# Performance work log

Hardware: AMD Instinct MI355X
Metric: run time of the kernel (lower is better)

Reference implementation:

```python
import jax, jax.numpy as jnp
import numpy as np

K = 10
ALPHA = 0.1

def setup_inputs() -> dict:
    key = jax.random.key(0)
    k1, k2, k3, k4 = jax.random.split(key, 4)
    N, E, IN, HID, OUT = 100000, 3200000, 512, 256, 64
    x = jax.random.normal(k1, (N, IN), dtype=jnp.float32)
    edge_index = jax.random.randint(k2, (2, E), 0, N, dtype=jnp.int64)
    W1 = jax.random.normal(k3, (IN, HID), dtype=jnp.float32) * (1.0 / np.sqrt(IN))
    b1 = jnp.zeros((HID,), jnp.float32)
    W2 = jax.random.normal(k4, (HID, OUT), dtype=jnp.float32) * (1.0 / np.sqrt(HID))
    b2 = jnp.zeros((OUT,), jnp.float32)
    return {"x": x, "edge_index": edge_index, "W1": W1, "b1": b1, "W2": W2, "b2": b2}

def reference(x, edge_index, W1, b1, W2, b2):
    N = x.shape[0]
    # gcn_norm with self-loops (PyG default for APPNP)
    loop = jnp.arange(N, dtype=edge_index.dtype)
    src = jnp.concatenate([edge_index[0], loop])  # [E+N]
    dst = jnp.concatenate([edge_index[1], loop])
    ones = jnp.ones(src.shape[0], dtype=x.dtype)
    deg = jax.ops.segment_sum(ones, dst, num_segments=N)
    dis = jnp.where(deg > 0, jax.lax.rsqrt(deg), 0.0)
    norm = dis[src] * dis[dst]  # [E+N]

    # 2-layer MLP (dropout disabled: eval mode)
    h = jnp.maximum(x @ W1 + b1, 0.0) @ W2 + b2  # [N, out]

    # K-step PPR diffusion: z <- alpha*h + (1-alpha)*A_hat z
    def step(z, _):
        agg = jax.ops.segment_sum(norm[:, None] * z[src], dst, num_segments=N)
        return ALPHA * h + (1.0 - ALPHA) * agg, None

    z, _ = jax.lax.scan(step, h, None, length=K)
    return jax.nn.log_softmax(z, axis=-1)
```

## Files before the change

### kernel.cpp

```cpp
#include <hip/hip_runtime.h>
#include <hip/hip_bf16.h>

#define ALPHA_F 0.1f
#define KSTEPS 10
#define BKT_SH 9
#define P1_CHUNK 8192
#define MAXPAD_PER_BUCKET (512 * 32)

typedef __attribute__((ext_vector_type(8))) short bf16x8;
typedef __attribute__((ext_vector_type(4))) float f32x4;

__device__ __forceinline__ unsigned short f2bf(float f) {
  union { float f; unsigned int u; } v; v.f = f;
  unsigned int u = v.u;
  u += 0x7FFFu + ((u >> 16) & 1u);
  return (unsigned short)(u >> 16);
}
__device__ __forceinline__ float bflo(unsigned int u) { return __uint_as_float(u << 16); }
__device__ __forceinline__ float bfhi(unsigned int u) { return __uint_as_float(u & 0xFFFF0000u); }

__device__ __forceinline__ void gload16(const void* g, void* l) {
  __builtin_amdgcn_global_load_lds(
      (const __attribute__((address_space(1))) void*)g,
      (__attribute__((address_space(3))) void*)l, 16, 0, 0);
}


__global__ __launch_bounds__(256)
void p0_hist(const int* __restrict__ dstv, int E, int* __restrict__ bhist) {
  __shared__ int h[256];
  int t = threadIdx.x;
  h[t] = 0;
  __syncthreads();
  int b0 = blockIdx.x * P1_CHUNK;
  int lim = min(P1_CHUNK, E - b0);
  for (int i = t; i < lim; i += 256) atomicAdd(&h[dstv[b0 + i] >> BKT_SH], 1);
  __syncthreads();
  if (h[t]) atomicAdd(&bhist[t], h[t]);
}

__global__ void p0_scan(const int* __restrict__ bhist, int* __restrict__ bbase,
                        int* __restrict__ gcur) {
  __shared__ int s[256];
  int t = threadIdx.x;
  int mine = bhist[t];
  s[t] = mine;
  __syncthreads();
  for (int off = 1; off < 256; off <<= 1) {
    int v = (t >= off) ? s[t - off] : 0;
    __syncthreads();
    s[t] += v;
    __syncthreads();
  }
  int excl = s[t] - mine;
  bbase[t] = excl;
  gcur[t] = excl;
}

__global__ __launch_bounds__(256)
void p1_scatter(const int* __restrict__ srcv, const int* __restrict__ dstv, int E,
                int* __restrict__ gcur, int2* __restrict__ tmp) {
  __shared__ int h[256];
  __shared__ int loc[256];
  int t = threadIdx.x;
  int b0 = blockIdx.x * P1_CHUNK;
  int lim = min(P1_CHUNK, E - b0);
  h[t] = 0;
  __syncthreads();
  for (int i = t; i < lim; i += 256) atomicAdd(&h[dstv[b0 + i] >> BKT_SH], 1);
  __syncthreads();
  loc[t] = h[t] ? atomicAdd(&gcur[t], h[t]) : 0;
  __syncthreads();
  h[t] = 0;
  __syncthreads();
  for (int i = t; i < lim; i += 256) {
    int d = dstv[b0 + i], s = srcv[b0 + i];
    int b = d >> BKT_SH;
    int pos = loc[b] + atomicAdd(&h[b], 1);
    tmp[pos] = make_int2(s, d);
  }
}

__global__ __launch_bounds__(256)
void p2_bucket(const int2* __restrict__ tmp, const int* __restrict__ bbase,
               const int* __restrict__ bhist, int* __restrict__ counts,
               int* __restrict__ rowptr, int* __restrict__ col, int N) {
  __shared__ int h1[512];
  __shared__ int cur[512];
  __shared__ int s2[256];
  const int t = threadIdx.x;
  const int b = blockIdx.x;
  const int base = bbase[b];
  const int pbase = base + b * MAXPAD_PER_BUCKET;
  const int sz = bhist[b];
  const int r0 = b << BKT_SH;
  const int nrows = min(512, N - r0);

  h1[t] = 0; h1[t + 256] = 0;
  __syncthreads();
  for (int i = t; i < sz; i += 256) atomicAdd(&h1[tmp[base + i].y - r0], 1);
  __syncthreads();
  int a = (h1[2 * t] + 31) & ~31;
  int c = (h1[2 * t + 1] + 31) & ~31;
  s2[t] = a + c;
  __syncthreads();
  for (int off = 1; off < 256; off <<= 1) {
    int v = (t >= off) ? s2[t - off] : 0;
    __syncthreads();
    s2[t] += v;
    __syncthreads();
  }
  int excl2 = s2[t] - (a + c);
  cur[2 * t] = excl2;
  cur[2 * t + 1] = excl2 + a;
  __syncthreads();
  if (t < nrows)       { rowptr[r0 + t] = pbase + cur[t];             counts[r0 + t] = h1[t]; }
  if (t + 256 < nrows) { rowptr[r0 + t + 256] = pbase + cur[t + 256]; counts[r0 + t + 256] = h1[t + 256]; }
  __syncthreads();
  for (int i = t; i < sz; i += 256) {
    int2 e = tmp[base + i];
    int p = pbase + atomicAdd(&cur[e.y - r0], 1);
    col[p] = e.x;
  }
  __syncthreads();
  for (int i = t; i < nrows; i += 256) {
    int cnt = h1[i];
    int c32 = (cnt + 31) & ~31;
    int ps = pbase + cur[i];
    for (int k = cnt; k < c32; ++k) col[ps++] = N;
  }
}

__global__ void k_dis(const int* __restrict__ counts, float* __restrict__ dis, int N) {
  int i = blockIdx.x * 256 + threadIdx.x;
  if (i < N) dis[i] = rsqrtf((float)(counts[i] + 1));
}

__global__ void k_zrow(unsigned short* __restrict__ yA, unsigned short* __restrict__ yB, int N) {
  int t = threadIdx.x;
  if (t < 64) yA[(size_t)N * 64 + t] = 0;
  else        yB[(size_t)N * 64 + (t - 64)] = 0;
}

__global__ void k_wconv1(const float* __restrict__ W, unsigned short* __restrict__ WT) {
  int idx = blockIdx.x * 256 + threadIdx.x;
  if (idx >= 512 * 256) return;
  int e = idx & 7, n = (idx >> 3) & 15, q = (idx >> 7) & 7;
  int nsub = (idx >> 10) & 15, kstep = idx >> 14;
  int k = kstep * 64 + q * 8 + e;
  int ncol = nsub * 16 + n;
  WT[idx] = f2bf(W[(size_t)k * 256 + ncol]);
}

__global__ void k_wconv2(const float* __restrict__ W, unsigned short* __restrict__ WT) {
  int idx = blockIdx.x * 256 + threadIdx.x;
  if (idx >= 256 * 64) return;
  int e = idx & 7, n = (idx >> 3) & 15, q = (idx >> 7) & 7;
  int nsub = (idx >> 10) & 3, kstep = idx >> 12;
  int k = kstep * 64 + q * 8 + e;
  int ncol = nsub * 16 + n;
  WT[idx] = f2bf(W[(size_t)k * 64 + ncol]);
}

__global__ __launch_bounds__(512)
void gemm1_kernel(const float* __restrict__ X, const unsigned short* __restrict__ Bt,
                  const float* __restrict__ bias, unsigned short* __restrict__ outT,
                  int M) {
  __shared__ __align__(16) unsigned short Al[8192];
  __shared__ __align__(16) unsigned short Bl[16384];
  const int t = threadIdx.x;
  const int m0 = blockIdx.x * 128;
  const int lane = t & 63;
  const int w = t >> 6;
  const int wm = w >> 2, wn = w & 3;

  const int sm = ((t >> 7) << 4) + (t & 15);
  const int sq = (t >> 4) & 7;
  const int r1 = m0 + sm;
  const int r2 = r1 + 64;
  const bool g1 = r1 < M, g2 = r2 < M;

  f32x4 acc[4][4] = {};

  for (int ks = 0; ks < 8; ++ks) {
    const int kc = ks * 64 + sq * 8;
    uint4 v1 = {0, 0, 0, 0}, v2 = {0, 0, 0, 0};
    if (g1) {
      const float* p = X + (size_t)r1 * 512 + kc;
      float4 a = *(const float4*)p, b = *(const float4*)(p + 4);
      unsigned short* o = (unsigned short*)&v1;
      o[0] = f2bf(a.x); o[1] = f2bf(a.y); o[2] = f2bf(a.z); o[3] = f2bf(a.w);
      o[4] = f2bf(b.x); o[5] = f2bf(b.y); o[6] = f2bf(b.z); o[7] = f2bf(b.w);
    }
    if (g2) {
      const float* p = X + (size_t)r2 * 512 + kc;
      float4 a = *(const float4*)p, b = *(const float4*)(p + 4);
      unsigned short* o = (unsigned short*)&v2;
      o[0] = f2bf(a.x); o[1] = f2bf(a.y); o[2] = f2bf(a.z); o[3] = f2bf(a.w);
      o[4] = f2bf(b.x); o[5] = f2bf(b.y); o[6] = f2bf(b.z); o[7] = f2bf(b.w);
    }
    *(uint4*)&Al[t * 8] = v1;
    *(uint4*)&Al[(t + 512) * 8] = v2;

    const unsigned short* bs = Bt + ks * 16384;
    gload16(bs + (size_t)t * 8,          &Bl[t * 8]);
    gload16(bs + (size_t)(t + 512) * 8,  &Bl[(t + 512) * 8]);
    gload16(bs + (size_t)(t + 1024) * 8, &Bl[(t + 1024) * 8]);
    gload16(bs + (size_t)(t + 1536) * 8, &Bl[(t + 1536) * 8]);
    __syncthreads();

#pragma unroll
    for (int kk = 0; kk < 2; ++kk) {
      bf16x8 af[4], bfv[4];
#pragma unroll
      for (int mi = 0; mi < 4; ++mi)
        af[mi] = *(const bf16x8*)&Al[((wm * 4 + mi) * 128 + kk * 64 + (lane >> 4) * 16 + (lane & 15)) * 8];
#pragma unroll
      for (int ni = 0; ni < 4; ++ni)
        bfv[ni] = *(const bf16x8*)&Bl[((wn * 4 + ni) * 128 + kk * 64 + (lane >> 4) * 16 + (lane & 15)) * 8];
#pragma unroll
      for (int mi = 0; mi < 4; ++mi)
#pragma unroll
        for (int ni = 0; ni < 4; ++ni)
          acc[mi][ni] = __builtin_amdgcn_mfma_f32_16x16x32_bf16(af[mi], bfv[ni], acc[mi][ni], 0, 0, 0);
    }
    __syncthreads();
  }

  unsigned short* ob = outT + (size_t)blockIdx.x * 32768;
#pragma unroll
  for (int mi = 0; mi < 4; ++mi) {
#pragma unroll
    for (int ni = 0; ni < 4; ++ni) {
      int n = wn * 64 + ni * 16 + (lane & 15);
      float bv = bias[n];
      int kstep = n >> 6, q = (n >> 3) & 7, e = n & 7;
#pragma unroll
      for (int j = 0; j < 4; ++j) {
        int lm = wm * 64 + mi * 16 + (lane >> 4) * 4 + j;
        if (m0 + lm < M) {
          float v = fmaxf(acc[mi][ni][j] + bv, 0.f);
          int msub = lm >> 4, mm = lm & 15;
          ob[((((kstep * 8 + msub) * 8 + q) * 16 + mm) * 8) + e] = f2bf(v);
        }
      }
    }
  }
}

__global__ __launch_bounds__(256)
void gemm2_kernel(const unsigned short* __restrict__ At, const unsigned short* __restrict__ Bt,
                  const float* __restrict__ bias, const float* __restrict__ dis,
                  unsigned short* __restrict__ hb, unsigned short* __restrict__ y0, int M) {
  __shared__ __align__(16) unsigned short Al[8192];
  __shared__ __align__(16) unsigned short Bl[4096];
  const int t = threadIdx.x;
  const int m0 = blockIdx.x * 128;
  const int lane = t & 63;
  const int w = t >> 6;
  const int wm = w >> 1, wn = w & 1;

  f32x4 acc[4][2] = {};

  const unsigned short* ab = At + (size_t)blockIdx.x * 32768;
  for (int ks = 0; ks < 4; ++ks) {
    const unsigned short* as = ab + ks * 8192;
    gload16(as + (size_t)t * 8,         &Al[t * 8]);
    gload16(as + (size_t)(t + 256) * 8, &Al[(t + 256) * 8]);
    gload16(as + (size_t)(t + 512) * 8, &Al[(t + 512) * 8]);
    gload16(as + (size_t)(t + 768) * 8, &Al[(t + 768) * 8]);
    const unsigned short* bs = Bt + ks * 4096;
    gload16(bs + (size_t)t * 8,         &Bl[t * 8]);
    gload16(bs + (size_t)(t + 256) * 8, &Bl[(t + 256) * 8]);
    __syncthreads();

#pragma unroll
    for (int kk = 0; kk < 2; ++kk) {
      bf16x8 af[4], bfv[2];
#pragma unroll
      for (int mi = 0; mi < 4; ++mi)
        af[mi] = *(const bf16x8*)&Al[((wm * 4 + mi) * 128 + kk * 64 + (lane >> 4) * 16 + (lane & 15)) * 8];
#pragma unroll
      for (int ni = 0; ni < 2; ++ni)
        bfv[ni] = *(const bf16x8*)&Bl[((wn * 2 + ni) * 128 + kk * 64 + (lane >> 4) * 16 + (lane & 15)) * 8];
#pragma unroll
      for (int mi = 0; mi < 4; ++mi)
#pragma unroll
        for (int ni = 0; ni < 2; ++ni)
          acc[mi][ni] = __builtin_amdgcn_mfma_f32_16x16x32_bf16(af[mi], bfv[ni], acc[mi][ni], 0, 0, 0);
    }
    __syncthreads();
  }

#pragma unroll
  for (int mi = 0; mi < 4; ++mi) {
#pragma unroll
    for (int ni = 0; ni < 2; ++ni) {
      int gn = wn * 32 + ni * 16 + (lane & 15);
      float bv = bias[gn];
#pragma unroll
      for (int j = 0; j < 4; ++j) {
        int gm = m0 + wm * 64 + mi * 16 + (lane >> 4) * 4 + j;
        if (gm < M) {
          float v = acc[mi][ni][j] + bv;
          hb[(size_t)gm * 64 + gn] = f2bf(v);
          y0[(size_t)gm * 64 + gn] = f2bf(dis[gm] * v);
        }
      }
    }
  }
}

template<bool FINAL>
__global__ __launch_bounds__(256)
void prop_kernel(const unsigned short* __restrict__ yin,
                 const unsigned short* __restrict__ hb,
                 void* __restrict__ yout,
                 const int* __restrict__ rowptr, const int* __restrict__ counts,
                 const int* __restrict__ col, const float* __restrict__ dis, int N) {
  int wid = (blockIdx.x * 256 + threadIdx.x) >> 6;
  wid = __builtin_amdgcn_readfirstlane(wid);
  if (wid >= N) return;
  const int lane = threadIdx.x & 63;
  const int g = lane >> 3;
  const int lg = lane & 7;
  const int r = wid;

  const int start = rowptr[r];
  const int cnt = counts[r];
  const int iters = (cnt + 31) >> 5;
  const float dr = dis[r];
  uint4 zs = *(const uint4*)(yin + (size_t)r * 64 + 8 * lg);
  uint4 hr = *(const uint4*)(hb + (size_t)r * 64 + 8 * lg);

  float acc[8] = {0.f, 0.f, 0.f, 0.f, 0.f, 0.f, 0.f, 0.f};
  const int* cp = col + start + 4 * g;
  for (int it = 0; it < iters; ++it, cp += 32) {
    int4 cc = *(const int4*)cp;
    uint4 z0 = *(const uint4*)(yin + (size_t)cc.x * 64 + 8 * lg);
    uint4 z1 = *(const uint4*)(yin + (size_t)cc.y * 64 + 8 * lg);
    uint4 z2 = *(const uint4*)(yin + (size_t)cc.z * 64 + 8 * lg);
    uint4 z3 = *(const uint4*)(yin + (size_t)cc.w * 64 + 8 * lg);
    acc[0] += bflo(z0.x); acc[1] += bfhi(z0.x); acc[2] += bflo(z0.y); acc[3] += bfhi(z0.y);
    acc[4] += bflo(z0.z); acc[5] += bfhi(z0.z); acc[6] += bflo(z0.w); acc[7] += bfhi(z0.w);
    acc[0] += bflo(z1.x); acc[1] += bfhi(z1.x); acc[2] += bflo(z1.y); acc[3] += bfhi(z1.y);
    acc[4] += bflo(z1.z); acc[5] += bfhi(z1.z); acc[6] += bflo(z1.w); acc[7] += bfhi(z1.w);
    acc[0] += bflo(z2.x); acc[1] += bfhi(z2.x); acc[2] += bflo(z2.y); acc[3] += bfhi(z2.y);
    acc[4] += bflo(z2.z); acc[5] += bfhi(z2.z); acc[6] += bflo(z2.w); acc[7] += bfhi(z2.w);
    acc[0] += bflo(z3.x); acc[1] += bfhi(z3.x); acc[2] += bflo(z3.y); acc[3] += bfhi(z3.y);
    acc[4] += bflo(z3.z); acc[5] += bfhi(z3.z); acc[6] += bflo(z3.w); acc[7] += bfhi(z3.w);
  }
#pragma unroll
  for (int k = 0; k < 8; ++k) {
    acc[k] += __shfl_xor(acc[k], 8);
    acc[k] += __shfl_xor(acc[k], 16);
    acc[k] += __shfl_xor(acc[k], 32);
  }

  float selfz[8] = { bflo(zs.x), bfhi(zs.x), bflo(zs.y), bfhi(zs.y),
                     bflo(zs.z), bfhi(zs.z), bflo(zs.w), bfhi(zs.w) };
  float hv[8]    = { bflo(hr.x), bfhi(hr.x), bflo(hr.y), bfhi(hr.y),
                     bflo(hr.z), bfhi(hr.z), bflo(hr.w), bfhi(hr.w) };
  float f[8];
#pragma unroll
  for (int k = 0; k < 8; ++k)
    f[k] = ALPHA_F * hv[k] + (1.f - ALPHA_F) * dr * (acc[k] + selfz[k]);

  if (!FINAL) {
    if (g == 0) {
      uint4 o;
      o.x = (unsigned)f2bf(dr * f[0]) | ((unsigned)f2bf(dr * f[1]) << 16);
      o.y = (unsigned)f2bf(dr * f[2]) | ((unsigned)f2bf(dr * f[3]) << 16);
      o.z = (unsigned)f2bf(dr * f[4]) | ((unsigned)f2bf(dr * f[5]) << 16);
      o.w = (unsigned)f2bf(dr * f[6]) | ((unsigned)f2bf(dr * f[7]) << 16);
      *(uint4*)((unsigned short*)yout + (size_t)r * 64 + 8 * lg) = o;
    }
  } else {
    float m = f[0];
#pragma unroll
    for (int k = 1; k < 8; ++k) m = fmaxf(m, f[k]);
    m = fmaxf(m, __shfl_xor(m, 1));
    m = fmaxf(m, __shfl_xor(m, 2));
    m = fmaxf(m, __shfl_xor(m, 4));
    float s = 0.f;
#pragma unroll
    for (int k = 0; k < 8; ++k) s += __expf(f[k] - m);
    s += __shfl_xor(s, 1);
    s += __shfl_xor(s, 2);
    s += __shfl_xor(s, 4);
    float ls = __logf(s);
    if (g == 0) {
      float* op = (float*)yout + (size_t)r * 64 + 8 * lg;
      *(float4*)op       = make_float4(f[0] - m - ls, f[1] - m - ls, f[2] - m - ls, f[3] - m - ls);
      *(float4*)(op + 4) = make_float4(f[4] - m - ls, f[5] - m - ls, f[6] - m - ls, f[7] - m - ls);
    }
  }
}

extern "C" void kernel_launch(void* const* d_in, const int* in_sizes, int n_in,
                              void* d_out, int out_size, void* d_ws, size_t ws_size,
                              hipStream_t stream) {
  const float* x  = (const float*)d_in[0];
  const int*   ei = (const int*)d_in[1];
  const float* W1 = (const float*)d_in[2];
  const float* b1 = (const float*)d_in[3];
  const float* W2 = (const float*)d_in[4];
  const float* b2 = (const float*)d_in[5];

  const int IN = 512, HID = 256, OUT = 64;
  const int N = in_sizes[0] / IN;
  const int E = in_sizes[1] / 2;
  const int* srcv = ei;
  const int* dstv = ei + E;
  const int NBUCK = (N + (1 << BKT_SH) - 1) >> BKT_SH;
  const int MT = (N + 127) / 128;
  const size_t N1 = (size_t)N + 1;

  char* p = (char*)d_ws;
  auto alloc = [&](size_t bytes) -> void* {
    void* r = (void*)p;
    p += (bytes + 255) & ~(size_t)255;
    return r;
  };
  int*   bhist  = (int*)alloc(256 * 4);
  int*   bbase  = (int*)alloc(256 * 4);
  int*   gcur   = (int*)alloc(256 * 4);
  int*   counts = (int*)alloc((size_t)N * 4);
  float* dis    = (float*)alloc((size_t)N * 4);
  int*   rowptr = (int*)alloc((size_t)(N + 1) * 4);
  int*   col    = (int*)alloc(((size_t)E + 256 * MAXPAD_PER_BUCKET) * 4);
  unsigned short* WT1t = (unsigned short*)alloc((size_t)IN * HID * 2);
  unsigned short* WT2t = (unsigned short*)alloc((size_t)HID * OUT * 2);
  unsigned short* hb   = (unsigned short*)alloc((size_t)N * OUT * 2);
  unsigned short* yA   = (unsigned short*)alloc(N1 * OUT * 2);
  size_t hidT_bytes = (size_t)MT * 32768 * 2;
  size_t R_bytes = hidT_bytes;
  if ((size_t)E * 8 > R_bytes) R_bytes = (size_t)E * 8;
  if (N1 * OUT * 2 > R_bytes) R_bytes = N1 * OUT * 2;
  char* R = (char*)alloc(R_bytes);
  int2* tmp = (int2*)R;
  unsigned short* hidT = (unsigned short*)R;
  unsigned short* yB = (unsigned short*)R;

  hipMemsetAsync(bhist, 0, 256 * 4, stream);

  const int p1blocks = (E + P1_CHUNK - 1) / P1_CHUNK;
  p0_hist<<<p1blocks, 256, 0, stream>>>(dstv, E, bhist);
  p0_scan<<<1, 256, 0, stream>>>(bhist, bbase, gcur);
  p1_scatter<<<p1blocks, 256, 0, stream>>>(srcv, dstv, E, gcur, tmp);
  p2_bucket<<<NBUCK, 256, 0, stream>>>(tmp, bbase, bhist, counts, rowptr, col, N);
  k_dis<<<(N + 255) / 256, 256, 0, stream>>>(counts, dis, N);

  k_wconv1<<<(IN * HID + 255) / 256, 256, 0, stream>>>(W1, WT1t);
  k_wconv2<<<(HID * OUT + 255) / 256, 256, 0, stream>>>(W2, WT2t);

  gemm1_kernel<<<MT, 512, 0, stream>>>(x, WT1t, b1, hidT, N);
  gemm2_kernel<<<MT, 256, 0, stream>>>(hidT, WT2t, b2, dis, hb, yA, N);
  k_zrow<<<1, 128, 0, stream>>>(yA, yB, N);

  const int pblocks = (N + 3) / 4;
  const unsigned short* ycur = yA;
  for (int it = 0; it < KSTEPS - 1; ++it) {
    unsigned short* ynext = (it & 1) ? yA : yB;
    prop_kernel<false><<<pblocks, 256, 0, stream>>>(ycur, hb, ynext, rowptr, counts, col, dis, N);
    ycur = ynext;
  }
  prop_kernel<true><<<pblocks, 256, 0, stream>>>(ycur, hb, d_out, rowptr, counts, col, dis, N);
}
```

Before: 764.8 us.

## Split feature dim into XCD-local halves, pack edge temp, fuse dis into bucketing

```diff
diff --git a/kernel.cpp b/kernel.cpp
--- a/kernel.cpp
+++ b/kernel.cpp
@@ -5,7 +5,7 @@
 #define KSTEPS 10
 #define BKT_SH 9
 #define P1_CHUNK 8192
-#define MAXPAD_PER_BUCKET (512 * 32)
+#define MAXPAD_PER_BUCKET (512 * 16)
 
 typedef __attribute__((ext_vector_type(8))) short bf16x8;
 typedef __attribute__((ext_vector_type(4))) float f32x4;
@@ -59,7 +59,7 @@
 
 __global__ __launch_bounds__(256)
 void p1_scatter(const int* __restrict__ srcv, const int* __restrict__ dstv, int E,
-                int* __restrict__ gcur, int2* __restrict__ tmp) {
+                int* __restrict__ gcur, int* __restrict__ tmp) {
   __shared__ int h[256];
   __shared__ int loc[256];
   int t = threadIdx.x;
@@ -77,14 +77,15 @@
     int d = dstv[b0 + i], s = srcv[b0 + i];
     int b = d >> BKT_SH;
     int pos = loc[b] + atomicAdd(&h[b], 1);
-    tmp[pos] = make_int2(s, d);
-  }
-}
-
-__global__ __launch_bounds__(256)
-void p2_bucket(const int2* __restrict__ tmp, const int* __restrict__ bbase,
+    tmp[pos] = (s << BKT_SH) | (d & 511);
+  }
+}
+
+__global__ __launch_bounds__(256)
+void p2_bucket(const int* __restrict__ tmp, const int* __restrict__ bbase,
                const int* __restrict__ bhist, int* __restrict__ counts,
-               int* __restrict__ rowptr, int* __restrict__ col, int N) {
+               float* __restrict__ dis, int* __restrict__ rowptr,
+               int* __restrict__ col, int N) {
   __shared__ int h1[512];
   __shared__ int cur[512];
   __shared__ int s2[256];
@@ -98,10 +99,10 @@
 
   h1[t] = 0; h1[t + 256] = 0;
   __syncthreads();
-  for (int i = t; i < sz; i += 256) atomicAdd(&h1[tmp[base + i].y - r0], 1);
-  __syncthreads();
-  int a = (h1[2 * t] + 31) & ~31;
-  int c = (h1[2 * t + 1] + 31) & ~31;
+  for (int i = t; i < sz; i += 256) atomicAdd(&h1[tmp[base + i] & 511], 1);
+  __syncthreads();
+  int a = (h1[2 * t] + 15) & ~15;
+  int c = (h1[2 * t + 1] + 15) & ~15;
   s2[t] = a + c;
   __syncthreads();
   for (int off = 1; off < 256; off <<= 1) {
@@ -114,32 +115,36 @@
   cur[2 * t] = excl2;
   cur[2 * t + 1] = excl2 + a;
   __syncthreads();
-  if (t < nrows)       { rowptr[r0 + t] = pbase + cur[t];             counts[r0 + t] = h1[t]; }
-  if (t + 256 < nrows) { rowptr[r0 + t + 256] = pbase + cur[t + 256]; counts[r0 + t + 256] = h1[t + 256]; }
+  if (t < nrows) {
+    rowptr[r0 + t] = pbase + cur[t];
+    counts[r0 + t] = h1[t];
+    dis[r0 + t] = rsqrtf((float)(h1[t] + 1));
+  }
+  if (t + 256 < nrows) {
+    rowptr[r0 + t + 256] = pbase + cur[t + 256];
+    counts[r0 + t + 256] = h1[t + 256];
+    dis[r0 + t + 256] = rsqrtf((float)(h1[t + 256] + 1));
+  }
   __syncthreads();
   for (int i = t; i < sz; i += 256) {
-    int2 e = tmp[base + i];
-    int p = pbase + atomicAdd(&cur[e.y - r0], 1);
-    col[p] = e.x;
+    int u = tmp[base + i];
+    int p = pbase + atomicAdd(&cur[u & 511], 1);
+    col[p] = u >> BKT_SH;
   }
   __syncthreads();
   for (int i = t; i < nrows; i += 256) {
     int cnt = h1[i];
-    int c32 = (cnt + 31) & ~31;
+    int c16 = (cnt + 15) & ~15;
     int ps = pbase + cur[i];
-    for (int k = cnt; k < c32; ++k) col[ps++] = N;
-  }
-}
-
-__global__ void k_dis(const int* __restrict__ counts, float* __restrict__ dis, int N) {
-  int i = blockIdx.x * 256 + threadIdx.x;
-  if (i < N) dis[i] = rsqrtf((float)(counts[i] + 1));
+    for (int k = cnt; k < c16; ++k) col[ps++] = N;
+  }
 }
 
 __global__ void k_zrow(unsigned short* __restrict__ yA, unsigned short* __restrict__ yB, int N) {
   int t = threadIdx.x;
-  if (t < 64) yA[(size_t)N * 64 + t] = 0;
-  else        yB[(size_t)N * 64 + (t - 64)] = 0;
+  size_t N1 = (size_t)N + 1;
+  if (t < 64) yA[((size_t)(t >> 5) * N1 + N) * 32 + (t & 31)] = 0;
+  else { int u = t - 64; yB[((size_t)(u >> 5) * N1 + N) * 32 + (u & 31)] = 0; }
 }
 
 __global__ void k_wconv1(const float* __restrict__ W, unsigned short* __restrict__ WT) {
@@ -259,6 +264,7 @@
   const int lane = t & 63;
   const int w = t >> 6;
   const int wm = w >> 1, wn = w & 1;
+  const size_t N1 = (size_t)M + 1;
 
   f32x4 acc[4][2] = {};
 
@@ -298,13 +304,14 @@
     for (int ni = 0; ni < 2; ++ni) {
       int gn = wn * 32 + ni * 16 + (lane & 15);
       float bv = bias[gn];
+      int hh = gn >> 5, cc = gn & 31;
 #pragma unroll
       for (int j = 0; j < 4; ++j) {
         int gm = m0 + wm * 64 + mi * 16 + (lane >> 4) * 4 + j;
         if (gm < M) {
           float v = acc[mi][ni][j] + bv;
-          hb[(size_t)gm * 64 + gn] = f2bf(v);
-          y0[(size_t)gm * 64 + gn] = f2bf(dis[gm] * v);
+          hb[((size_t)hh * M + gm) * 32 + cc] = f2bf(v);
+          y0[((size_t)hh * N1 + gm) * 32 + cc] = f2bf(dis[gm] * v);
         }
       }
     }
@@ -314,44 +321,44 @@
 template<bool FINAL>
 __global__ __launch_bounds__(256)
 void prop_kernel(const unsigned short* __restrict__ yin,
-                 const unsigned short* __restrict__ hb,
+                 const unsigned short* __restrict__ hbh,
                  void* __restrict__ yout,
                  const int* __restrict__ rowptr, const int* __restrict__ counts,
-                 const int* __restrict__ col, const float* __restrict__ dis, int N) {
-  int wid = (blockIdx.x * 256 + threadIdx.x) >> 6;
-  wid = __builtin_amdgcn_readfirstlane(wid);
-  if (wid >= N) return;
+                 const int* __restrict__ col, const float* __restrict__ dis,
+                 int N, int G) {
+  const int bid = blockIdx.x;
+  const int xcd = bid & 7;
+  const int h = xcd >> 2;
+  const int i = (bid >> 3) * 4 + (xcd & 3);
+  if (i >= G) return;
+  int r = i * 4 + (threadIdx.x >> 6);
+  if (r >= N) return;
+  r = __builtin_amdgcn_readfirstlane(r);
   const int lane = threadIdx.x & 63;
-  const int g = lane >> 3;
-  const int lg = lane & 7;
-  const int r = wid;
+  const int g = lane >> 2;
+  const int sl = lane & 3;
+  const size_t N1 = (size_t)N + 1;
+  const unsigned short* yq = yin + (size_t)h * N1 * 32;
 
   const int start = rowptr[r];
-  const int cnt = counts[r];
-  const int iters = (cnt + 31) >> 5;
+  const int iters = (counts[r] + 15) >> 4;
   const float dr = dis[r];
-  uint4 zs = *(const uint4*)(yin + (size_t)r * 64 + 8 * lg);
-  uint4 hr = *(const uint4*)(hb + (size_t)r * 64 + 8 * lg);
+  uint4 zs = *(const uint4*)(yq + (size_t)r * 32 + sl * 8);
+  uint4 hr = *(const uint4*)(hbh + ((size_t)h * N + r) * 32 + sl * 8);
 
   float acc[8] = {0.f, 0.f, 0.f, 0.f, 0.f, 0.f, 0.f, 0.f};
-  const int* cp = col + start + 4 * g;
-  for (int it = 0; it < iters; ++it, cp += 32) {
-    int4 cc = *(const int4*)cp;
-    uint4 z0 = *(const uint4*)(yin + (size_t)cc.x * 64 + 8 * lg);
-    uint4 z1 = *(const uint4*)(yin + (size_t)cc.y * 64 + 8 * lg);
-    uint4 z2 = *(const uint4*)(yin + (size_t)cc.z * 64 + 8 * lg);
-    uint4 z3 = *(const uint4*)(yin + (size_t)cc.w * 64 + 8 * lg);
-    acc[0] += bflo(z0.x); acc[1] += bfhi(z0.x); acc[2] += bflo(z0.y); acc[3] += bfhi(z0.y);
-    acc[4] += bflo(z0.z); acc[5] += bfhi(z0.z); acc[6] += bflo(z0.w); acc[7] += bfhi(z0.w);
-    acc[0] += bflo(z1.x); acc[1] += bfhi(z1.x); acc[2] += bflo(z1.y); acc[3] += bfhi(z1.y);
-    acc[4] += bflo(z1.z); acc[5] += bfhi(z1.z); acc[6] += bflo(z1.w); acc[7] += bfhi(z1.w);
-    acc[0] += bflo(z2.x); acc[1] += bfhi(z2.x); acc[2] += bflo(z2.y); acc[3] += bfhi(z2.y);
-    acc[4] += bflo(z2.z); acc[5] += bfhi(z2.z); acc[6] += bflo(z2.w); acc[7] += bfhi(z2.w);
-    acc[0] += bflo(z3.x); acc[1] += bfhi(z3.x); acc[2] += bflo(z3.y); acc[3] += bfhi(z3.y);
-    acc[4] += bflo(z3.z); acc[5] += bfhi(z3.z); acc[6] += bflo(z3.w); acc[7] += bfhi(z3.w);
+  const int* cp = col + start + g;
+  for (int it = 0; it < iters; ++it) {
+    int c = cp[it * 16];
+    uint4 z = *(const uint4*)(yq + (size_t)c * 32 + sl * 8);
+    acc[0] += bflo(z.x); acc[1] += bfhi(z.x);
+    acc[2] += bflo(z.y); acc[3] += bfhi(z.y);
+    acc[4] += bflo(z.z); acc[5] += bfhi(z.z);
+    acc[6] += bflo(z.w); acc[7] += bfhi(z.w);
   }
 #pragma unroll
   for (int k = 0; k < 8; ++k) {
+    acc[k] += __shfl_xor(acc[k], 4);
     acc[k] += __shfl_xor(acc[k], 8);
     acc[k] += __shfl_xor(acc[k], 16);
     acc[k] += __shfl_xor(acc[k], 32);
@@ -373,28 +380,31 @@
       o.y = (unsigned)f2bf(dr * f[2]) | ((unsigned)f2bf(dr * f[3]) << 16);
       o.z = (unsigned)f2bf(dr * f[4]) | ((unsigned)f2bf(dr * f[5]) << 16);
       o.w = (unsigned)f2bf(dr * f[6]) | ((unsigned)f2bf(dr * f[7]) << 16);
-      *(uint4*)((unsigned short*)yout + (size_t)r * 64 + 8 * lg) = o;
+      *(uint4*)((unsigned short*)yout + ((size_t)h * N1 + r) * 32 + sl * 8) = o;
     }
   } else {
-    float m = f[0];
-#pragma unroll
-    for (int k = 1; k < 8; ++k) m = fmaxf(m, f[k]);
-    m = fmaxf(m, __shfl_xor(m, 1));
-    m = fmaxf(m, __shfl_xor(m, 2));
-    m = fmaxf(m, __shfl_xor(m, 4));
-    float s = 0.f;
-#pragma unroll
-    for (int k = 0; k < 8; ++k) s += __expf(f[k] - m);
-    s += __shfl_xor(s, 1);
-    s += __shfl_xor(s, 2);
-    s += __shfl_xor(s, 4);
-    float ls = __logf(s);
     if (g == 0) {
-      float* op = (float*)yout + (size_t)r * 64 + 8 * lg;
-      *(float4*)op       = make_float4(f[0] - m - ls, f[1] - m - ls, f[2] - m - ls, f[3] - m - ls);
-      *(float4*)(op + 4) = make_float4(f[4] - m - ls, f[5] - m - ls, f[6] - m - ls, f[7] - m - ls);
-    }
-  }
+      float* op = (float*)yout + (size_t)r * 64 + h * 32 + sl * 8;
+      *(float4*)op       = make_float4(f[0], f[1], f[2], f[3]);
+      *(float4*)(op + 4) = make_float4(f[4], f[5], f[6], f[7]);
+    }
+  }
+}
+
+__global__ __launch_bounds__(256)
+void k_lsm(float* __restrict__ z, int N) {
+  int r = (blockIdx.x * 256 + threadIdx.x) >> 6;
+  if (r >= N) return;
+  int lane = threadIdx.x & 63;
+  float v = z[(size_t)r * 64 + lane];
+  float m = v;
+#pragma unroll
+  for (int off = 32; off; off >>= 1) m = fmaxf(m, __shfl_xor(m, off));
+  float e = __expf(v - m);
+  float s = e;
+#pragma unroll
+  for (int off = 32; off; off >>= 1) s += __shfl_xor(s, off);
+  z[(size_t)r * 64 + lane] = v - m - __logf(s);
 }
 
 extern "C" void kernel_launch(void* const* d_in, const int* in_sizes, int n_in,
@@ -427,20 +437,19 @@
   int*   gcur   = (int*)alloc(256 * 4);
   int*   counts = (int*)alloc((size_t)N * 4);
   float* dis    = (float*)alloc((size_t)N * 4);
-  int*   rowptr = (int*)alloc((size_t)(N + 1) * 4);
+  int*   rowptr = (int*)alloc((size_t)N * 4);
   int*   col    = (int*)alloc(((size_t)E + 256 * MAXPAD_PER_BUCKET) * 4);
   unsigned short* WT1t = (unsigned short*)alloc((size_t)IN * HID * 2);
   unsigned short* WT2t = (unsigned short*)alloc((size_t)HID * OUT * 2);
   unsigned short* hb   = (unsigned short*)alloc((size_t)N * OUT * 2);
   unsigned short* yA   = (unsigned short*)alloc(N1 * OUT * 2);
+  unsigned short* yBs  = (unsigned short*)alloc(N1 * OUT * 2);
   size_t hidT_bytes = (size_t)MT * 32768 * 2;
   size_t R_bytes = hidT_bytes;
-  if ((size_t)E * 8 > R_bytes) R_bytes = (size_t)E * 8;
-  if (N1 * OUT * 2 > R_bytes) R_bytes = N1 * OUT * 2;
+  if ((size_t)E * 4 > R_bytes) R_bytes = (size_t)E * 4;
   char* R = (char*)alloc(R_bytes);
-  int2* tmp = (int2*)R;
+  int* tmp = (int*)R;
   unsigned short* hidT = (unsigned short*)R;
-  unsigned short* yB = (unsigned short*)R;
 
   hipMemsetAsync(bhist, 0, 256 * 4, stream);
 
@@ -448,22 +457,23 @@
   p0_hist<<<p1blocks, 256, 0, stream>>>(dstv, E, bhist);
   p0_scan<<<1, 256, 0, stream>>>(bhist, bbase, gcur);
   p1_scatter<<<p1blocks, 256, 0, stream>>>(srcv, dstv, E, gcur, tmp);
-  p2_bucket<<<NBUCK, 256, 0, stream>>>(tmp, bbase, bhist, counts, rowptr, col, N);
-  k_dis<<<(N + 255) / 256, 256, 0, stream>>>(counts, dis, N);
+  p2_bucket<<<NBUCK, 256, 0, stream>>>(tmp, bbase, bhist, counts, dis, rowptr, col, N);
 
   k_wconv1<<<(IN * HID + 255) / 256, 256, 0, stream>>>(W1, WT1t);
   k_wconv2<<<(HID * OUT + 255) / 256, 256, 0, stream>>>(W2, WT2t);
 
   gemm1_kernel<<<MT, 512, 0, stream>>>(x, WT1t, b1, hidT, N);
   gemm2_kernel<<<MT, 256, 0, stream>>>(hidT, WT2t, b2, dis, hb, yA, N);
-  k_zrow<<<1, 128, 0, stream>>>(yA, yB, N);
-
-  const int pblocks = (N + 3) / 4;
+  k_zrow<<<1, 128, 0, stream>>>(yA, yBs, N);
+
+  const int G = (N + 3) / 4;
+  const int pgrid = 8 * ((G + 3) / 4);
   const unsigned short* ycur = yA;
   for (int it = 0; it < KSTEPS - 1; ++it) {
-    unsigned short* ynext = (it & 1) ? yA : yB;
-    prop_kernel<false><<<pblocks, 256, 0, stream>>>(ycur, hb, ynext, rowptr, counts, col, dis, N);
+    unsigned short* ynext = (it & 1) ? yA : yBs;
+    prop_kernel<false><<<pgrid, 256, 0, stream>>>(ycur, hb, ynext, rowptr, counts, col, dis, N, G);
     ycur = ynext;
   }
-  prop_kernel<true><<<pblocks, 256, 0, stream>>>(ycur, hb, d_out, rowptr, counts, col, dis, N);
-}
+  prop_kernel<true><<<pgrid, 256, 0, stream>>>(ycur, hb, d_out, rowptr, counts, col, dis, N, G);
+  k_lsm<<<(N + 3) / 4, 256, 0, stream>>>((float*)d_out, N);
+}
```

Result: slower. 1.188 ms (+55.4%).
